# Optimization experiments

Hardware: AMD Instinct MI355X
Metric: run time of the kernel (lower is better)

The kernel has to match this reference:

```python
import jax, jax.numpy as jnp
import numpy as np

K_FUTURE = 3
GAMMA = 0.25
LAMBDA_CP = 0.1
EPS = 1e-08


def setup_inputs() -> dict:
    key = jax.random.key(0)
    ks = jax.random.split(key, 8)
    B, T, d, Kc = 64, 512, 1024, 256
    Z = jax.random.normal(ks[0], (B, T, d), dtype=jnp.float32)
    # torch init: uniform(-1/Kc, 1/Kc)
    codebook = jax.random.uniform(ks[1], (Kc, d), dtype=jnp.float32,
                                  minval=-1.0 / Kc, maxval=1.0 / Kc)
    s = 1.0 / np.sqrt(d)
    gru_Wih = jax.random.normal(ks[2], (3 * d, d), dtype=jnp.float32) * s
    gru_Whh = jax.random.normal(ks[3], (3 * d, d), dtype=jnp.float32) * s
    gru_bih = jnp.zeros((3 * d,), jnp.float32)
    gru_bhh = jnp.zeros((3 * d,), jnp.float32)
    proj_W = jax.random.normal(ks[4], (d, d), dtype=jnp.float32) * s
    proj_b = jnp.zeros((d,), jnp.float32)
    return {"Z": Z, "codebook": codebook, "gru_Wih": gru_Wih, "gru_Whh": gru_Whh,
            "gru_bih": gru_bih, "gru_bhh": gru_bhh, "proj_W": proj_W, "proj_b": proj_b}


def _gru(x, Wih, Whh, bih, bhh):
    # x: (B, T, d) -> hidden states (B, T, d); torch GRU gate math
    B, T, d = x.shape

    def step(h, xt):
        gi = xt @ Wih.T + bih
        gh = h @ Whh.T + bhh
        i_r, i_z, i_n = jnp.split(gi, 3, axis=-1)
        h_r, h_z, h_n = jnp.split(gh, 3, axis=-1)
        r = jax.nn.sigmoid(i_r + h_r)
        z = jax.nn.sigmoid(i_z + h_z)
        n = jnp.tanh(i_n + r * h_n)
        h_new = (1.0 - z) * n + z * h
        return h_new, h_new

    h0 = jnp.zeros((B, d), x.dtype)
    _, hs = jax.lax.scan(step, h0, jnp.swapaxes(x, 0, 1))
    return jnp.swapaxes(hs, 0, 1)


def _quantize(Z, codebook):
    B, T, d = Z.shape
    flat = Z.reshape(-1, d)                                   # (N, d)
    # squared euclidean distances; argmin identical to cdist(p=2)
    d2 = (jnp.sum(flat * flat, axis=1, keepdims=True)
          - 2.0 * flat @ codebook.T
          + jnp.sum(codebook * codebook, axis=1)[None, :])    # (N, Kc)
    idx = jnp.argmin(d2, axis=1)                              # (N,)
    quantized = codebook[idx].reshape(B, T, d)
    return quantized, idx.reshape(B, T)


def _context_loss(Z, quantized, gru_Wih, gru_Whh, gru_bih, gru_bhh, proj_W, proj_b):
    B, T, d = Z.shape
    hs = _gru(quantized, gru_Wih, gru_Whh, gru_bih, gru_bhh)
    h = hs @ proj_W.T + proj_b                                # (B, T, d)
    total = jnp.float32(0.0)
    for k in range(1, K_FUTURE + 1):
        if T <= k:
            continue
        hk = h[:, :T - k]                                     # (B, T-k, d)
        zk = Z[:, k:]                                         # (B, T-k, d)
        pos = jnp.einsum('btd,btd->bt', hk, zk)               # (B, T-k)
        # sum over tau of mean over batch
        pos_loss = jnp.sum(jnp.mean(-jnp.log(jax.nn.sigmoid(pos) + EPS), axis=0))
        # negatives use a random batch permutation; the mean over (b, c) is
        # permutation-invariant, so compute the full pairwise logits.
        neg = jnp.einsum('btd,ctd->tbc', hk, zk)              # (T-k, B, B)
        neg_loss = jnp.sum(jnp.mean(-jnp.log(1.0 - jax.nn.sigmoid(neg) + EPS), axis=(1, 2)))
        total = total + pos_loss + LAMBDA_CP * neg_loss
    if K_FUTURE > 0 and T > K_FUTURE:
        total = total / (K_FUTURE * (T - K_FUTURE))
    return total


def _vq_loss(Z, quantized):
    commitment = jnp.mean((jax.lax.stop_gradient(Z) - quantized) ** 2)
    codebook_l = jnp.mean((Z - jax.lax.stop_gradient(quantized)) ** 2)
    return commitment + GAMMA * codebook_l


def reference(Z, codebook, gru_Wih, gru_Whh, gru_bih, gru_bhh, proj_W, proj_b):
    quantized, indices = _quantize(Z, codebook)
    L_cp = _context_loss(Z, quantized, gru_Wih, gru_Whh, gru_bih, gru_bhh, proj_W, proj_b)
    L_vq = _vq_loss(Z, quantized)
    L_total = L_cp + L_vq
    return quantized, indices, L_total, L_cp, L_vq
```

## Files before the change

### kernel.cpp

```cpp
#include <hip/hip_runtime.h>
#include <hip/hip_bf16.h>

#define B_ 64
#define T_ 512
#define D_ 1024
#define NQ_ (B_*T_*D_)
#define NI_ (B_*T_)

typedef __attribute__((ext_vector_type(8))) short bf16x8;
typedef __attribute__((ext_vector_type(4))) float f32x4;

__device__ inline ushort f2bf(float f) {
    uint x = __float_as_uint(f);
    return (ushort)((x + 0x7FFFu + ((x >> 16) & 1u)) >> 16);
}
__device__ inline float bf2f(ushort u) { return __uint_as_float(((uint)u) << 16); }

__device__ __forceinline__ void astore64(ulong* p, ulong v) {
    __hip_atomic_store(p, v, __ATOMIC_RELAXED, __HIP_MEMORY_SCOPE_AGENT);
}

typedef const __attribute__((address_space(1))) void GV;
typedef __attribute__((address_space(3))) void LV;
__device__ __forceinline__ void gll16(const void* g, void* l) {
    __builtin_amdgcn_global_load_lds((GV*)g, (LV*)l, 16, 0, 0);
}

__device__ __forceinline__ float sigf(float x) { return 1.0f / (1.0f + __expf(-x)); }
__device__ __forceinline__ float tanhfast(float x) {
    float e = __expf(-2.0f * fabsf(x));
    float t = (1.0f - e) / (1.0f + e);
    return copysignf(t, x);
}

__global__ __launch_bounds__(256) void conv_kernel(const float* __restrict__ src,
                                                   ushort* __restrict__ dst, int n) {
    int i = (blockIdx.x * 256 + threadIdx.x) * 4;
    if (i >= n) return;
    float4 v = *reinterpret_cast<const float4*>(src + i);
    ushort4 o;
    o.x = f2bf(v.x); o.y = f2bf(v.y); o.z = f2bf(v.z); o.w = f2bf(v.w);
    *reinterpret_cast<ushort4*>(dst + i) = o;
}

__global__ __launch_bounds__(256) void whhfr_kernel(const float* __restrict__ Whh,
                                                    ushort* __restrict__ Whh_fr) {
    int l = threadIdx.x & 63;
    int unit = blockIdx.x * 4 + (threadIdx.x >> 6);
    int c = unit & 31;
    int g = (unit >> 5) % 3;
    int jb = unit / 96;
    int row = g * 1024 + jb * 16 + (l & 15);
    int k0 = c * 32 + (l >> 4) * 8;
    const float* s = Whh + (size_t)row * 1024 + k0;
    float4 f0 = *reinterpret_cast<const float4*>(s);
    float4 f1 = *reinterpret_cast<const float4*>(s + 4);
    uint4 pk;
    pk.x = (uint)f2bf(f0.x) | ((uint)f2bf(f0.y) << 16);
    pk.y = (uint)f2bf(f0.z) | ((uint)f2bf(f0.w) << 16);
    pk.z = (uint)f2bf(f1.x) | ((uint)f2bf(f1.y) << 16);
    pk.w = (uint)f2bf(f1.z) | ((uint)f2bf(f1.w) << 16);
    reinterpret_cast<uint4*>(Whh_fr)[(size_t)unit * 64 + l] = pk;
}

__device__ inline float np_pairwise_sq_1024(const float* a) {
    float L[8];
    for (int c = 0; c < 8; ++c) {
        const float* p = a + c * 128;
        float r[8];
        #pragma unroll
        for (int k = 0; k < 8; ++k) r[k] = __fmul_rn(p[k], p[k]);
        for (int i = 8; i < 128; i += 8) {
            #pragma unroll
            for (int k = 0; k < 8; ++k) {
                float v = p[i + k];
                r[k] = __fadd_rn(r[k], __fmul_rn(v, v));
            }
        }
        L[c] = __fadd_rn(__fadd_rn(__fadd_rn(r[0], r[1]), __fadd_rn(r[2], r[3])),
                         __fadd_rn(__fadd_rn(r[4], r[5]), __fadd_rn(r[6], r[7])));
    }
    return __fadd_rn(__fadd_rn(__fadd_rn(L[0], L[1]), __fadd_rn(L[2], L[3])),
                     __fadd_rn(__fadd_rn(L[4], L[5]), __fadd_rn(L[6], L[7])));
}

__global__ __launch_bounds__(256) void c2_kernel(const float* __restrict__ cb,
                                                 float* __restrict__ c2) {
    int j = threadIdx.x;
    c2[j] = np_pairwise_sq_1024(cb + (size_t)j * D_);
}

__global__ __launch_bounds__(256) void quantize_kernel(const float* __restrict__ Z,
                                                       const float* __restrict__ cb,
                                                       const float* __restrict__ c2,
                                                       float* __restrict__ qout,
                                                       float* __restrict__ idxout,
                                                       int* __restrict__ idxT) {
    __shared__ float rows[8][D_];
    __shared__ float z2s[8];
    __shared__ float d2s[256];
    __shared__ int   idxs[256];
    __shared__ int   bestIdx[8];
    int tid = threadIdx.x;
    size_t row0 = (size_t)blockIdx.x * 8;

    for (int p = 0; p < 8; ++p) {
        float4 v = *reinterpret_cast<const float4*>(Z + (row0 + p) * D_ + tid * 4);
        *reinterpret_cast<float4*>(&rows[p][tid * 4]) = v;
    }
    __syncthreads();

    if (tid < 8) z2s[tid] = np_pairwise_sq_1024(rows[tid]);

    float g2[8];
    #pragma unroll
    for (int r = 0; r < 8; ++r) g2[r] = 0.0f;
    const float* crow = cb + (size_t)tid * D_;
    for (int e = 0; e < D_; e += 4) {
        float4 cv = *reinterpret_cast<const float4*>(crow + e);
        #pragma unroll
        for (int r = 0; r < 8; ++r) {
            g2[r] = __fmaf_rn(__fmul_rn(2.0f, rows[r][e]),     cv.x, g2[r]);
            g2[r] = __fmaf_rn(__fmul_rn(2.0f, rows[r][e + 1]), cv.y, g2[r]);
            g2[r] = __fmaf_rn(__fmul_rn(2.0f, rows[r][e + 2]), cv.z, g2[r]);
            g2[r] = __fmaf_rn(__fmul_rn(2.0f, rows[r][e + 3]), cv.w, g2[r]);
        }
    }
    __syncthreads();

    for (int r = 0; r < 8; ++r) {
        d2s[tid] = __fadd_rn(__fsub_rn(z2s[r], g2[r]), c2[tid]);
        idxs[tid] = tid;
        __syncthreads();
        for (int s = 128; s > 0; s >>= 1) {
            if (tid < s) {
                float ov = d2s[tid + s]; int oi = idxs[tid + s];
                if (ov < d2s[tid] || (ov == d2s[tid] && oi < idxs[tid])) {
                    d2s[tid] = ov; idxs[tid] = oi;
                }
            }
            __syncthreads();
        }
        if (tid == 0) bestIdx[r] = idxs[0];
        __syncthreads();
    }

    if (tid < 8) {
        int row = (int)row0 + tid;
        idxout[row] = (float)bestIdx[tid];
        idxT[((row & 511) << 6) + (row >> 9)] = bestIdx[tid];
    }
    for (int r = 0; r < 8; ++r) {
        int bi = bestIdx[r];
        float4 v = *reinterpret_cast<const float4*>(cb + (size_t)bi * D_ + tid * 4);
        *reinterpret_cast<float4*>(qout + (row0 + r) * D_ + tid * 4) = v;
    }
}

__global__ __launch_bounds__(256) void gmat_kernel(const float* __restrict__ cb,
                                                   const float* __restrict__ Wih,
                                                   const float* __restrict__ bih,
                                                   const float* __restrict__ bhh,
                                                   ushort* __restrict__ Gp) {
    int m0 = blockIdx.x * 64;
    int n0 = blockIdx.y * 64;
    __shared__ ushort As[64][136];
    __shared__ ushort Bs[64][136];
    int tid = threadIdx.x;
    int w = tid >> 6, l = tid & 63, lr = l & 15, lk = l >> 4;
    f32x4 acc[4];
    #pragma unroll
    for (int i = 0; i < 4; ++i) acc[i] = f32x4{0.f, 0.f, 0.f, 0.f};

    for (int kc = 0; kc < D_; kc += 128) {
        for (int v = tid; v < 2048; v += 256) {
            int r = (v >> 4) & 63, kp = (v & 15) << 3;
            const float* src = (v < 1024) ? (cb  + (size_t)(m0 + r) * D_ + kc + kp)
                                          : (Wih + (size_t)(n0 + r) * D_ + kc + kp);
            float4 f0 = *reinterpret_cast<const float4*>(src);
            float4 f1 = *reinterpret_cast<const float4*>(src + 4);
            uint4 pk;
            pk.x = (uint)f2bf(f0.x) | ((uint)f2bf(f0.y) << 16);
            pk.y = (uint)f2bf(f0.z) | ((uint)f2bf(f0.w) << 16);
            pk.z = (uint)f2bf(f1.x) | ((uint)f2bf(f1.y) << 16);
            pk.w = (uint)f2bf(f1.z) | ((uint)f2bf(f1.w) << 16);
            ushort* dst = (v < 1024) ? &As[r][kp] : &Bs[r][kp];
            *reinterpret_cast<uint4*>(dst) = pk;
        }
        __syncthreads();
        #pragma unroll
        for (int kk = 0; kk < 4; ++kk) {
            bf16x8 bb = *reinterpret_cast<const bf16x8*>(&Bs[(w << 4) + lr][(kk << 5) + (lk << 3)]);
            #pragma unroll
            for (int mi = 0; mi < 4; ++mi) {
                bf16x8 a = *reinterpret_cast<const bf16x8*>(&As[(mi << 4) + lr][(kk << 5) + (lk << 3)]);
                acc[mi] = __builtin_amdgcn_mfma_f32_16x16x32_bf16(a, bb, acc[mi], 0, 0, 0);
            }
        }
        __syncthreads();
    }
    int n = n0 + (w << 4) + lr;
    int gate = n >> 10, jj = n & 1023;
    float bias = bih[n] + (gate < 2 ? bhh[n] : 0.0f);
    #pragma unroll
    for (int mi = 0; mi < 4; ++mi)
        #pragma unroll
        for (int reg = 0; reg < 4; ++reg) {
            int m = m0 + (mi << 4) + (lk << 2) + reg;
            Gp[((((size_t)m << 10) | jj) << 2) + gate] = f2bf(acc[mi][reg] + bias);
        }
}

__global__ __launch_bounds__(256, 1) void recur_kernel(
    const ushort* __restrict__ Whh_fr,
    const ushort* __restrict__ Gp,
    const int*    __restrict__ idxT,
    const float*  __restrict__ bhh,
    ushort* h_hist,
    uint*   flags)
{
    extern __shared__ ushort dynlds[];
    const int tid = threadIdx.x, blk = blockIdx.x;
    const int w = tid >> 6, l = tid & 63;
    const int lr = l & 15, lk = l >> 4;
    const int j0 = blk << 4;
    const int b  = (w << 4) + lr;
    const int jq = j0 + (lk << 2);
    const ushort* Bbase = Whh_fr + (size_t)blk * 49152;
    ushort* myfrag = dynlds + (w << 14);
    const int rowoff = (((w << 4) + lr) << 10) + (lk << 3);
    const float4 bhhn4 = *reinterpret_cast<const float4*>(&bhh[2048 + jq]);
    const float* bhhn = (const float*)&bhhn4;
    float hfp[4] = {0.f, 0.f, 0.f, 0.f};
    bool dead = false;

    for (int t = 0; t < T_; ++t) {
        const ushort* src = h_hist + ((size_t)(t == 0 ? 512 : t - 1) << 16) + rowoff;
        #pragma unroll
        for (int c = 0; c < 32; ++c)
            gll16(src + (c << 5), myfrag + (c << 9));

        const int ci = idxT[(t << 6) + b];
        const uint4* gpv = reinterpret_cast<const uint4*>(Gp + ((((size_t)ci << 10) | jq) << 2));
        uint4 ga = gpv[0], gb2 = gpv[1];
        ushort gp16[16];
        *reinterpret_cast<uint4*>(&gp16[0]) = ga;
        *reinterpret_cast<uint4*>(&gp16[8]) = gb2;

        asm volatile("s_waitcnt vmcnt(0)" ::: "memory");
        __builtin_amdgcn_sched_barrier(0);

        f32x4 acc0 = {0.f,0.f,0.f,0.f}, acc1 = acc0, acc2 = acc0;
        #pragma unroll 8
        for (int c = 0; c < 32; ++c) {
            bf16x8 hfr = *reinterpret_cast<const bf16x8*>(myfrag + (c << 9) + (l << 3));
            bf16x8 w0 = *reinterpret_cast<const bf16x8*>(Bbase +         (c << 9) + (l << 3));
            bf16x8 w1 = *reinterpret_cast<const bf16x8*>(Bbase + 16384 + (c << 9) + (l << 3));
            bf16x8 w2 = *reinterpret_cast<const bf16x8*>(Bbase + 32768 + (c << 9) + (l << 3));
            acc0 = __builtin_amdgcn_mfma_f32_16x16x32_bf16(w0, hfr, acc0, 0, 0, 0);
            acc1 = __builtin_amdgcn_mfma_f32_16x16x32_bf16(w1, hfr, acc1, 0, 0, 0);
            acc2 = __builtin_amdgcn_mfma_f32_16x16x32_bf16(w2, hfr, acc2, 0, 0, 0);
        }

        ushort4 hs;
        ushort* hsp = (ushort*)&hs;
        #pragma unroll
        for (int reg = 0; reg < 4; ++reg) {
            float rr = sigf(bf2f(gp16[reg * 4 + 0]) + acc0[reg]);
            float zz = sigf(bf2f(gp16[reg * 4 + 1]) + acc1[reg]);
            float nn = tanhfast(bf2f(gp16[reg * 4 + 2]) + rr * (acc2[reg] + bhhn[reg]));
            float hn = (1.0f - zz) * nn + zz * hfp[reg];
            hfp[reg] = hn;
            hsp[reg] = f2bf(hn);
        }
        astore64(reinterpret_cast<ulong*>(h_hist + ((size_t)t << 16) + (b << 10) + jq),
                 *reinterpret_cast<ulong*>(&hs));

        if (t < T_ - 1) {
            __syncthreads();
            if (tid == 0)
                __hip_atomic_store(&flags[blk << 4], (uint)(t + 1),
                                   __ATOMIC_RELAXED, __HIP_MEMORY_SCOPE_AGENT);
            if (w == 0 && !dead) {
                uint spins = 0;
                float pump = 1.0f;
                for (;;) {
                    uint f = __hip_atomic_load(&flags[l << 4], __ATOMIC_RELAXED,
                                               __HIP_MEMORY_SCOPE_AGENT);
                    if (__all(f >= (uint)(t + 1))) break;
                    #pragma unroll
                    for (int q = 0; q < 16; ++q)
                        pump = __fmaf_rn(pump, 1.0000001f, 0.0000001f);
                    asm volatile("" :: "v"(pump));
                    if (++spins > (1u << 20)) { dead = true; break; }
                }
            }
            __syncthreads();
        }
    }
}

__global__ __launch_bounds__(256) void proj_gemm_kernel(const ushort* __restrict__ h_hist,
                                                        const ushort* __restrict__ projW_bf,
                                                        const float* __restrict__ projb,
                                                        ushort* __restrict__ hproj,
                                                        int ch) {
    int t = ch * 256 + blockIdx.x;
    int n0 = blockIdx.y * 64;
    __shared__ ushort As[64][136];
    __shared__ ushort Bs[64][136];
    int tid = threadIdx.x;
    int w = tid >> 6, l = tid & 63, lr = l & 15, lk = l >> 4;
    f32x4 acc[4];
    #pragma unroll
    for (int i = 0; i < 4; ++i) acc[i] = f32x4{0.f,0.f,0.f,0.f};

    for (int kc = 0; kc < D_; kc += 128) {
        for (int v = tid; v < 2048; v += 256) {
            int r = (v >> 4) & 63, kp = (v & 15) << 3;
            if (v < 1024)
                *reinterpret_cast<uint4*>(&As[r][kp]) =
                    *reinterpret_cast<const uint4*>(h_hist + ((size_t)t << 16) + ((size_t)r << 10) + kc + kp);
            else
                *reinterpret_cast<uint4*>(&Bs[r][kp]) =
                    *reinterpret_cast<const uint4*>(projW_bf + ((size_t)(n0 + r) << 10) + kc + kp);
        }
        __syncthreads();
        #pragma unroll
        for (int kk = 0; kk < 4; ++kk) {
            bf16x8 bb = *reinterpret_cast<const bf16x8*>(&Bs[(w << 4) + lr][(kk << 5) + (lk << 3)]);
            #pragma unroll
            for (int mi = 0; mi < 4; ++mi) {
                bf16x8 a = *reinterpret_cast<const bf16x8*>(&As[(mi << 4) + lr][(kk << 5) + (lk << 3)]);
                acc[mi] = __builtin_amdgcn_mfma_f32_16x16x32_bf16(a, bb, acc[mi], 0, 0, 0);
            }
        }
        __syncthreads();
    }
    int n = n0 + (w << 4) + lr;
    float pb = projb[n];
    #pragma unroll
    for (int mi = 0; mi < 4; ++mi)
        #pragma unroll
        for (int reg = 0; reg < 4; ++reg) {
            int b = (mi << 4) + (lk << 2) + reg;
            hproj[((size_t)(t & 255) << 16) + (b << 10) + n] = f2bf(acc[mi][reg] + pb);
        }
}

__global__ __launch_bounds__(256) void cpc_loss_kernel(const ushort* __restrict__ hproj,
                                                       const float* __restrict__ Z,
                                                       double* __restrict__ cp_sum,
                                                       int ch) {
    int tp = ch * 256 + blockIdx.x;
    int k = blockIdx.y + 1;
    if (tp >= T_ - k) return;
    __shared__ float Hs[64][33];
    __shared__ float Zs[64][33];
    int tid = threadIdx.x;
    int tx = tid & 15, ty = tid >> 4;
    float acc[4][4] = {};
    const ushort* Hbase = hproj + ((size_t)(tp & 255) << 16);
    const float* Zbase = Z + (size_t)(tp + k) * D_;
    const size_t zstride = (size_t)T_ * D_;
    int r = tid >> 3, c = (tid & 7) << 2;

    for (int kc = 0; kc < D_; kc += 32) {
        #pragma unroll
        for (int p = 0; p < 2; ++p) {
            int rr2 = r + 32 * p;
            ushort4 hv = *reinterpret_cast<const ushort4*>(Hbase + (size_t)rr2 * D_ + kc + c);
            float4 zv = *reinterpret_cast<const float4*>(Zbase + (size_t)rr2 * zstride + kc + c);
            Hs[rr2][c] = bf2f(hv.x); Hs[rr2][c+1] = bf2f(hv.y);
            Hs[rr2][c+2] = bf2f(hv.z); Hs[rr2][c+3] = bf2f(hv.w);
            Zs[rr2][c] = zv.x; Zs[rr2][c+1] = zv.y; Zs[rr2][c+2] = zv.z; Zs[rr2][c+3] = zv.w;
        }
        __syncthreads();
        #pragma unroll
        for (int kk = 0; kk < 32; ++kk) {
            float av[4], bv[4];
            #pragma unroll
            for (int i = 0; i < 4; ++i) av[i] = Hs[ty + 16*i][kk];
            #pragma unroll
            for (int jv = 0; jv < 4; ++jv) bv[jv] = Zs[tx + 16*jv][kk];
            #pragma unroll
            for (int i = 0; i < 4; ++i)
                #pragma unroll
                for (int jv = 0; jv < 4; ++jv)
                    acc[i][jv] = __fmaf_rn(av[i], bv[jv], acc[i][jv]);
        }
        __syncthreads();
    }

    double lsum = 0.0;
    #pragma unroll
    for (int i = 0; i < 4; ++i) {
        #pragma unroll
        for (int jv = 0; jv < 4; ++jv) {
            int bb = ty + 16*i, cc2 = tx + 16*jv;
            double v = (double)acc[i][jv];
            double sg = 1.0 / (1.0 + exp(-v));
            lsum += (0.1 / 4096.0) * (-log(1.0 - sg + 1e-8));
            if (bb == cc2) lsum += (1.0 / 64.0) * (-log(sg + 1e-8));
        }
    }
    __shared__ double red[256];
    red[tid] = lsum; __syncthreads();
    for (int s2 = 128; s2 > 0; s2 >>= 1) {
        if (tid < s2) red[tid] += red[tid + s2];
        __syncthreads();
    }
    if (tid == 0) atomicAdd(cp_sum, red[0]);
}

__global__ __launch_bounds__(256) void vq_kernel(const float* __restrict__ Z,
                                                 const float* __restrict__ Q,
                                                 double* __restrict__ vq_sum) {
    size_t i0 = ((size_t)blockIdx.x * 256 + threadIdx.x) * 4;
    const size_t stride = (size_t)2048 * 256 * 4;
    double s = 0.0;
    for (size_t i = i0; i < (size_t)NQ_; i += stride) {
        float4 z = *reinterpret_cast<const float4*>(Z + i);
        float4 q = *reinterpret_cast<const float4*>(Q + i);
        double d0 = (double)z.x - (double)q.x;
        double d1 = (double)z.y - (double)q.y;
        double d2 = (double)z.z - (double)q.z;
        double d3 = (double)z.w - (double)q.w;
        s += d0*d0 + d1*d1 + d2*d2 + d3*d3;
    }
    __shared__ double red[256];
    int tid = threadIdx.x;
    red[tid] = s; __syncthreads();
    for (int k = 128; k > 0; k >>= 1) {
        if (tid < k) red[tid] += red[tid + k];
        __syncthreads();
    }
    if (tid == 0) atomicAdd(vq_sum, red[0]);
}

__global__ void finalize_kernel(const double* __restrict__ accum,
                                float* __restrict__ scal) {
    double cp = accum[0] / 1527.0;
    double vq = accum[1] * 1.25 / (double)NQ_;
    scal[0] = (float)(cp + vq);
    scal[1] = (float)cp;
    scal[2] = (float)vq;
}

extern "C" void kernel_launch(void* const* d_in, const int* in_sizes, int n_in,
                              void* d_out, int out_size, void* d_ws, size_t ws_size,
                              hipStream_t stream) {
    const float* Z     = (const float*)d_in[0];
    const float* cb    = (const float*)d_in[1];
    const float* Wih   = (const float*)d_in[2];
    const float* Whh   = (const float*)d_in[3];
    const float* bih   = (const float*)d_in[4];
    const float* bhh   = (const float*)d_in[5];
    const float* projW = (const float*)d_in[6];
    const float* projb = (const float*)d_in[7];

    float* out       = (float*)d_out;
    float* quantized = out;
    float* idxout    = out + (size_t)NQ_;
    float* scal      = out + (size_t)NQ_ + NI_;

    char* p = (char*)d_ws;
    ushort* Whh_fr   = (ushort*)p;  p += 6291456;
    ushort* projW_bf = (ushort*)p;  p += 2097152;
    ushort* Gp       = (ushort*)p;  p += 2097152;
    int*    idxT     = (int*)p;     p += 131072;
    float*  c2f      = (float*)p;   p += 4096;
    char*   ctrl     = p;           p += 8192;
    ushort* h_hist   = (ushort*)p;  p += (size_t)513 * 131072;
    ushort* hproj    = (ushort*)p;  p += (size_t)256 * 131072;

    uint*   flags = (uint*)ctrl;
    double* accum = (double*)(ctrl + 4096);

    hipMemsetAsync(ctrl, 0, 8192, stream);
    hipMemsetAsync(h_hist + ((size_t)512 << 16), 0, 131072, stream);

    conv_kernel<<<1024, 256, 0, stream>>>(projW, projW_bf, 1048576);
    whhfr_kernel<<<1536, 256, 0, stream>>>(Whh, Whh_fr);
    c2_kernel<<<1, 256, 0, stream>>>(cb, c2f);
    quantize_kernel<<<4096, 256, 0, stream>>>(Z, cb, c2f, quantized, idxout, idxT);
    gmat_kernel<<<dim3(4, 48), 256, 0, stream>>>(cb, Wih, bih, bhh, Gp);

    hipFuncSetAttribute(reinterpret_cast<const void*>(recur_kernel),
                        hipFuncAttributeMaxDynamicSharedMemorySize, 131072);
    recur_kernel<<<dim3(64), dim3(256), 131072, stream>>>(Whh_fr, Gp, idxT, bhh,
                                                          h_hist, flags);

    for (int ch = 0; ch < 2; ++ch) {
        proj_gemm_kernel<<<dim3(256, 16), 256, 0, stream>>>(h_hist, projW_bf, projb, hproj, ch);
        cpc_loss_kernel<<<dim3(256, 3), 256, 0, stream>>>(hproj, Z, &accum[0], ch);
    }

    vq_kernel<<<2048, 256, 0, stream>>>(Z, quantized, &accum[1]);
    finalize_kernel<<<1, 1, 0, stream>>>(accum, scal);
}
```

Measured before the change: 6.925 ms.

## Fuse VQ loss into quantize kernel and simplify recurrence spin-wait

The VQ squared-error sum now accumulates inside the quantize kernel, using the Z rows already held in shared memory and the selected codebook rows. This removes the separate vq_kernel pass that re-read Z and the quantized output. The recurrence kernel fully unrolls its MFMA loop and changes the inter-block wait so every thread polls a flag, with no wave-0-only pump loop. The new wait adds many more concurrent atomic loads per block, which may raise contention on the flag lines.

```diff
diff --git a/kernel.cpp b/kernel.cpp
--- a/kernel.cpp
+++ b/kernel.cpp
@@ -95,12 +95,14 @@
                                                        const float* __restrict__ c2,
                                                        float* __restrict__ qout,
                                                        float* __restrict__ idxout,
-                                                       int* __restrict__ idxT) {
+                                                       int* __restrict__ idxT,
+                                                       double* __restrict__ vq_sum) {
     __shared__ float rows[8][D_];
     __shared__ float z2s[8];
     __shared__ float d2s[256];
     __shared__ int   idxs[256];
     __shared__ int   bestIdx[8];
+    __shared__ double redv[256];
     int tid = threadIdx.x;
     size_t row0 = (size_t)blockIdx.x * 8;
 
@@ -150,11 +152,25 @@
         idxout[row] = (float)bestIdx[tid];
         idxT[((row & 511) << 6) + (row >> 9)] = bestIdx[tid];
     }
+
+    double vqp = 0.0;
     for (int r = 0; r < 8; ++r) {
         int bi = bestIdx[r];
         float4 v = *reinterpret_cast<const float4*>(cb + (size_t)bi * D_ + tid * 4);
         *reinterpret_cast<float4*>(qout + (row0 + r) * D_ + tid * 4) = v;
-    }
+        const float* zr = &rows[r][tid * 4];
+        double d0 = (double)zr[0] - (double)v.x;
+        double d1 = (double)zr[1] - (double)v.y;
+        double d2 = (double)zr[2] - (double)v.z;
+        double d3 = (double)zr[3] - (double)v.w;
+        vqp += d0*d0 + d1*d1 + d2*d2 + d3*d3;
+    }
+    redv[tid] = vqp; __syncthreads();
+    for (int s = 128; s > 0; s >>= 1) {
+        if (tid < s) redv[tid] += redv[tid + s];
+        __syncthreads();
+    }
+    if (tid == 0) atomicAdd(vq_sum, redv[0]);
 }
 
 __global__ __launch_bounds__(256) void gmat_kernel(const float* __restrict__ cb,
@@ -228,7 +244,7 @@
     const int jq = j0 + (lk << 2);
     const ushort* Bbase = Whh_fr + (size_t)blk * 49152;
     ushort* myfrag = dynlds + (w << 14);
-    const int rowoff = (((w << 4) + lr) << 10) + (lk << 3);
+    const int rowoff = (b << 10) + (lk << 3);
     const float4 bhhn4 = *reinterpret_cast<const float4*>(&bhh[2048 + jq]);
     const float* bhhn = (const float*)&bhhn4;
     float hfp[4] = {0.f, 0.f, 0.f, 0.f};
@@ -251,7 +267,7 @@
         __builtin_amdgcn_sched_barrier(0);
 
         f32x4 acc0 = {0.f,0.f,0.f,0.f}, acc1 = acc0, acc2 = acc0;
-        #pragma unroll 8
+        #pragma unroll
         for (int c = 0; c < 32; ++c) {
             bf16x8 hfr = *reinterpret_cast<const bf16x8*>(myfrag + (c << 9) + (l << 3));
             bf16x8 w0 = *reinterpret_cast<const bf16x8*>(Bbase +         (c << 9) + (l << 3));
@@ -281,17 +297,10 @@
             if (tid == 0)
                 __hip_atomic_store(&flags[blk << 4], (uint)(t + 1),
                                    __ATOMIC_RELAXED, __HIP_MEMORY_SCOPE_AGENT);
-            if (w == 0 && !dead) {
+            if (!dead) {
                 uint spins = 0;
-                float pump = 1.0f;
-                for (;;) {
-                    uint f = __hip_atomic_load(&flags[l << 4], __ATOMIC_RELAXED,
-                                               __HIP_MEMORY_SCOPE_AGENT);
-                    if (__all(f >= (uint)(t + 1))) break;
-                    #pragma unroll
-                    for (int q = 0; q < 16; ++q)
-                        pump = __fmaf_rn(pump, 1.0000001f, 0.0000001f);
-                    asm volatile("" :: "v"(pump));
+                while (__hip_atomic_load(&flags[(tid & 63) << 4], __ATOMIC_RELAXED,
+                                         __HIP_MEMORY_SCOPE_AGENT) < (uint)(t + 1)) {
                     if (++spins > (1u << 20)) { dead = true; break; }
                 }
             }
@@ -413,31 +422,6 @@
     if (tid == 0) atomicAdd(cp_sum, red[0]);
 }
 
-__global__ __launch_bounds__(256) void vq_kernel(const float* __restrict__ Z,
-                                                 const float* __restrict__ Q,
-                                                 double* __restrict__ vq_sum) {
-    size_t i0 = ((size_t)blockIdx.x * 256 + threadIdx.x) * 4;
-    const size_t stride = (size_t)2048 * 256 * 4;
-    double s = 0.0;
-    for (size_t i = i0; i < (size_t)NQ_; i += stride) {
-        float4 z = *reinterpret_cast<const float4*>(Z + i);
-        float4 q = *reinterpret_cast<const float4*>(Q + i);
-        double d0 = (double)z.x - (double)q.x;
-        double d1 = (double)z.y - (double)q.y;
-        double d2 = (double)z.z - (double)q.z;
-        double d3 = (double)z.w - (double)q.w;
-        s += d0*d0 + d1*d1 + d2*d2 + d3*d3;
-    }
-    __shared__ double red[256];
-    int tid = threadIdx.x;
-    red[tid] = s; __syncthreads();
-    for (int k = 128; k > 0; k >>= 1) {
-        if (tid < k) red[tid] += red[tid + k];
-        __syncthreads();
-    }
-    if (tid == 0) atomicAdd(vq_sum, red[0]);
-}
-
 __global__ void finalize_kernel(const double* __restrict__ accum,
                                 float* __restrict__ scal) {
     double cp = accum[0] / 1527.0;
@@ -483,7 +467,8 @@
     conv_kernel<<<1024, 256, 0, stream>>>(projW, projW_bf, 1048576);
     whhfr_kernel<<<1536, 256, 0, stream>>>(Whh, Whh_fr);
     c2_kernel<<<1, 256, 0, stream>>>(cb, c2f);
-    quantize_kernel<<<4096, 256, 0, stream>>>(Z, cb, c2f, quantized, idxout, idxT);
+    quantize_kernel<<<4096, 256, 0, stream>>>(Z, cb, c2f, quantized, idxout, idxT,
+                                              &accum[1]);
     gmat_kernel<<<dim3(4, 48), 256, 0, stream>>>(cb, Wih, bih, bhh, Gp);
 
     hipFuncSetAttribute(reinterpret_cast<const void*>(recur_kernel),
@@ -496,6 +481,5 @@
         cpc_loss_kernel<<<dim3(256, 3), 256, 0, stream>>>(hproj, Z, &accum[0], ch);
     }
 
-    vq_kernel<<<2048, 256, 0, stream>>>(Z, quantized, &accum[1]);
     finalize_kernel<<<1, 1, 0, stream>>>(accum, scal);
 }
```

Result: faster. 6.401 ms (-7.6%).
